# Kernel tuning notes

Hardware: AMD Instinct MI355X
Metric: run time of the kernel (lower is better)

Reference implementation:

```python
import jax, jax.numpy as jnp
import numpy as np

B, DIN, H, NACT = 8192, 1025, 1024, 1026
NHEAD = 513  # npatches + STOP
K = 32       # kR = kS


def _make_seq(key, batch, n, k):
    k_idx, k_len = jax.random.split(key)
    # distinct indices per row: top-k of a random permutation
    perm = jnp.argsort(jax.random.uniform(k_idx, (batch, n)), axis=1)[:, :k]
    seq_len = jax.random.randint(k_len, (batch,), 1, k + 1).astype(jnp.int32)
    mask = jnp.arange(k)[None, :] < seq_len[:, None]
    seq_idx = jnp.where(mask, perm, -1).astype(jnp.int32)
    return seq_idx, seq_len


def setup_inputs() -> dict:
    key = jax.random.key(0)
    ks = jax.random.split(key, 8)
    state = jax.random.normal(ks[0], (B, DIN), dtype=jnp.float32)
    W0 = jax.random.normal(ks[1], (DIN, H), dtype=jnp.float32) * (2.0 / DIN) ** 0.5
    b0 = jnp.zeros((H,), jnp.float32)
    W1 = jax.random.normal(ks[2], (H, H), dtype=jnp.float32) * (2.0 / H) ** 0.5
    b1 = jnp.zeros((H,), jnp.float32)
    W2 = jax.random.normal(ks[3], (H, NACT), dtype=jnp.float32) * 0.01
    b2 = jnp.zeros((NACT,), jnp.float32)
    seq_idx_R, seq_len_R = _make_seq(ks[4], B, NHEAD, K)
    seq_idx_S, seq_len_S = _make_seq(ks[5], B, NHEAD, K)
    return {"state": state, "W0": W0, "b0": b0, "W1": W1, "b1": b1,
            "W2": W2, "b2": b2,
            "seq_idx_R": seq_idx_R, "seq_len_R": seq_len_R,
            "seq_idx_S": seq_idx_S, "seq_len_S": seq_len_S}


def _mlp(state, W0, b0, W1, b1, W2, b2):
    h = jax.nn.relu(state @ W0 + b0)
    h = jax.nn.relu(h @ W1 + b1)
    return h @ W2 + b2  # (B, NACT) logits


def _logprob_entropy_wo_replacement(logits, seq_idx, seq_len):
    # Faithful vectorized version of logprob_entropy_wo_replacement_batched.
    bsz, n = logits.shape
    col = jnp.arange(n)[None, :]
    neg_inf = jnp.float32(-jnp.inf)

    def step(carry, xs):
        remaining, logp, ent = carry          # (B,N) bool, (B,), (B,)
        t, idx_t = xs                          # scalar, (B,)
        active = t < seq_len                   # (B,)
        masked_logits = jnp.where(remaining, logits, neg_inf)
        lp = jax.nn.log_softmax(masked_logits, axis=-1)
        p = jnp.exp(lp)
        mp = jnp.where(remaining, p, 0.0)
        mlp_ = jnp.where(remaining, lp, 0.0)
        ent_step = -jnp.sum(mp * mlp_, axis=-1)
        ent = ent + jnp.where(active, ent_step, 0.0)
        valid = active & (idx_t >= 0)
        idx_safe = jnp.where(valid, idx_t, 0)
        g = jnp.take_along_axis(lp, idx_safe[:, None], axis=1)[:, 0]
        logp = logp + jnp.where(valid, g, 0.0)
        hit = (col == idx_safe[:, None]) & valid[:, None]
        remaining = remaining & ~hit
        return (remaining, logp, ent), None

    init = (jnp.ones((bsz, n), bool), jnp.zeros((bsz,), jnp.float32),
            jnp.zeros((bsz,), jnp.float32))
    ts = jnp.arange(seq_idx.shape[1], dtype=jnp.int32)
    (_, logp, ent), _ = jax.lax.scan(step, init, (ts, seq_idx.T))
    return logp, ent


def reference(state, W0, b0, W1, b1, W2, b2,
              seq_idx_R, seq_len_R, seq_idx_S, seq_len_S):
    x = _mlp(state, W0, b0, W1, b1, W2, b2)
    logpR, entR = _logprob_entropy_wo_replacement(x[:, :NHEAD], seq_idx_R, seq_len_R)
    logpS, entS = _logprob_entropy_wo_replacement(x[:, NHEAD:NHEAD + NHEAD], seq_idx_S, seq_len_S)
    # rows: [total logprob, total entropy] as in get_log_prob's (logpR+logpS, entR+entS)
    return jnp.stack([logpR + logpS, entR + entS], axis=0)  # (2, B)
```

## Files before the change

kernel.cpp:

```cpp
#include <hip/hip_runtime.h>
#include <cstdint>
#include <cstddef>

#define BATCH 8192
#define DIN   1025
#define HID   1024
#define NACT  1026
#define NHEAD 513
#define KSEL  32
#define KP0   1088
#define LGN   1024

typedef unsigned short u16;
typedef short bf16x8 __attribute__((ext_vector_type(8)));
typedef float f32x4 __attribute__((ext_vector_type(4)));

__device__ __forceinline__ u16 f2bf(float f) {
  unsigned u = __float_as_uint(f);
  u += 0x7fff + ((u >> 16) & 1);
  return (u16)(u >> 16);
}
__device__ __forceinline__ float bf2f(u16 h) {
  return __uint_as_float((unsigned)h << 16);
}

__device__ __forceinline__ void async_cp16(const u16* g, u16* l) {
  __builtin_amdgcn_global_load_lds((const __attribute__((address_space(1))) void*)g,
                                   (__attribute__((address_space(3))) void*)l,
                                   16, 0, 0);
}

__global__ __launch_bounds__(512) void k_cvt(const float* __restrict__ state,
    const float* __restrict__ W0, const float* __restrict__ W1,
    const float* __restrict__ W2,
    u16* __restrict__ As, u16* __restrict__ W0t, u16* __restrict__ W1t,
    u16* __restrict__ W2t, u16* __restrict__ W2c) {
  const int tid = threadIdx.x;
  const int b = blockIdx.x;
  {
    int i = b * 512 + tid;
    const int QPR = KP0 / 4;
    int r = i / QPR, c4 = (i - r * QPR) * 4;
    const float* src = state + (size_t)r * DIN + c4;
    ushort4 o;
    if (c4 + 3 < DIN) {
      o.x = f2bf(src[0]); o.y = f2bf(src[1]); o.z = f2bf(src[2]); o.w = f2bf(src[3]);
    } else {
      o.x = (c4 + 0 < DIN) ? f2bf(src[0]) : 0;
      o.y = (c4 + 1 < DIN) ? f2bf(src[1]) : 0;
      o.z = (c4 + 2 < DIN) ? f2bf(src[2]) : 0;
      o.w = (c4 + 3 < DIN) ? f2bf(src[3]) : 0;
    }
    *(ushort4*)(As + (size_t)r * KP0 + c4) = o;
  }
  if (b >= 3137) return;
  if (b == 3136) {
    for (int e = tid; e < 2048; e += 512) {
      int j = e >> 10, k = e & 1023;
      W2c[e] = f2bf(W2[(size_t)k * NACT + 1024 + j]);
    }
    return;
  }
  const float* W; u16* Wt; int K, ldW, Kp, tt = b;
  if (tt < 1088)      { W = W0; Wt = W0t; K = DIN; ldW = HID;  Kp = KP0; }
  else if (tt < 2112) { tt -= 1088; W = W1; Wt = W1t; K = HID; ldW = HID;  Kp = HID; }
  else                { tt -= 2112; W = W2; Wt = W2t; K = HID; ldW = NACT; Kp = HID; }
  int n0 = (tt & 31) * 32, k0 = (tt >> 5) * 32;
  __shared__ float tile[32][33];
  const int tx = tid & 31, ty = tid >> 5;
#pragma unroll
  for (int i = 0; i < 32; i += 16) {
    int k = k0 + ty + i;
    tile[ty + i][tx] = (k < K) ? W[(size_t)k * ldW + n0 + tx] : 0.f;
  }
  __syncthreads();
#pragma unroll
  for (int i = 0; i < 32; i += 16)
    Wt[(size_t)(n0 + ty + i) * Kp + k0 + tx] = f2bf(tile[tx][ty + i]);
}

template<bool RELU, int K>
__global__ __launch_bounds__(512, 1)
void gemm_bt(const u16* __restrict__ A, const u16* __restrict__ Bt,
             const float* __restrict__ bias, u16* __restrict__ Cout, int ldc)
{
  __shared__ __align__(16) u16 lds[73728];

  const int d = blockIdx.x;
  const int wg    = (d & 7) * 32 + (d >> 3);
  const int mtile = wg >> 3;
  const int ntile = wg & 7;
  const size_t bm = (size_t)mtile * 256;
  const size_t bn = (size_t)ntile * 128;

  const int tid  = threadIdx.x;
  const int wave = tid >> 6;
  const int lane = tid & 63;
  const int waveM = wave >> 1, waveN = wave & 1;
  const int lr = lane & 15, lq = lane >> 4;
  const int xr = lr & 7;

  const int row0 = tid >> 3;
  const int g_   = (tid & 7) ^ ((tid >> 3) & 7);
  const u16* gA0 = A  + (bm + row0)       * (size_t)K + g_ * 8;
  const u16* gA1 = A  + (bm + row0 + 64)  * (size_t)K + g_ * 8;
  const u16* gA2 = A  + (bm + row0 + 128) * (size_t)K + g_ * 8;
  const u16* gA3 = A  + (bm + row0 + 192) * (size_t)K + g_ * 8;
  const u16* gB0 = Bt + (bn + row0)       * (size_t)K + g_ * 8;
  const u16* gB1 = Bt + (bn + row0 + 64)  * (size_t)K + g_ * 8;

  auto stage = [&](int k0, int wb) {
    u16* a = lds + wb * 24576 + wave * 512;
    u16* b = a + 16384;
    async_cp16(gA0 + k0, a);
    async_cp16(gA1 + k0, a + 4096);
    async_cp16(gA2 + k0, a + 8192);
    async_cp16(gA3 + k0, a + 12288);
    async_cp16(gB0 + k0, b);
    async_cp16(gB1 + k0, b + 4096);
  };

  const int offA = (waveM * 64 + lr) * 64;
  const int offB = 16384 + (waveN * 64 + lr) * 64;
  const int s0 = ( lq      ^ xr) * 8;
  const int s1 = ((4 | lq) ^ xr) * 8;

  f32x4 acc[4][4] = {};
  bf16x8 af[4], bfr[4];

  const int NIT = K / 64;
  stage(0, 0);
  stage(64, 1);
  asm volatile("s_waitcnt vmcnt(6)" ::: "memory");
  __builtin_amdgcn_s_barrier();

  int rb = 0;
  for (int t = 0; t < NIT; ++t) {
    const int ro = rb * 24576;
    const bool pf = (t + 2 < NIT);

#pragma unroll
    for (int nf = 0; nf < 4; ++nf) bfr[nf] = *(const bf16x8*)(lds + ro + offB + nf * 1024 + s0);
#pragma unroll
    for (int mf = 0; mf < 4; ++mf) af[mf]  = *(const bf16x8*)(lds + ro + offA + mf * 1024 + s0);
    if (pf) {
      int wb = rb - 1; if (wb < 0) wb = 2;
      stage((t + 2) * 64, wb);
    }
    __builtin_amdgcn_s_barrier();
    asm volatile("s_waitcnt lgkmcnt(0)" ::: "memory");
    __builtin_amdgcn_sched_barrier(0);
    __builtin_amdgcn_s_setprio(1);
#pragma unroll
    for (int mf = 0; mf < 4; ++mf)
#pragma unroll
      for (int nf = 0; nf < 4; ++nf)
        acc[mf][nf] = __builtin_amdgcn_mfma_f32_16x16x32_bf16(af[mf], bfr[nf], acc[mf][nf], 0, 0, 0);
    __builtin_amdgcn_s_setprio(0);
    __builtin_amdgcn_s_barrier();

#pragma unroll
    for (int nf = 0; nf < 4; ++nf) bfr[nf] = *(const bf16x8*)(lds + ro + offB + nf * 1024 + s1);
#pragma unroll
    for (int mf = 0; mf < 4; ++mf) af[mf]  = *(const bf16x8*)(lds + ro + offA + mf * 1024 + s1);
    __builtin_amdgcn_s_barrier();
    asm volatile("s_waitcnt lgkmcnt(0)" ::: "memory");
    __builtin_amdgcn_sched_barrier(0);
    __builtin_amdgcn_s_setprio(1);
#pragma unroll
    for (int mf = 0; mf < 4; ++mf)
#pragma unroll
      for (int nf = 0; nf < 4; ++nf)
        acc[mf][nf] = __builtin_amdgcn_mfma_f32_16x16x32_bf16(af[mf], bfr[nf], acc[mf][nf], 0, 0, 0);
    __builtin_amdgcn_s_setprio(0);
    if (pf)               asm volatile("s_waitcnt vmcnt(6)" ::: "memory");
    else if (t + 1 < NIT) asm volatile("s_waitcnt vmcnt(0)" ::: "memory");
    __builtin_amdgcn_s_barrier();

    rb = (rb == 2) ? 0 : rb + 1;
  }

#pragma unroll
  for (int mf = 0; mf < 4; ++mf) {
    size_t rw = bm + waveM * 64 + mf * 16 + lq * 4;
#pragma unroll
    for (int nf = 0; nf < 4; ++nf) {
      int col = (int)bn + waveN * 64 + nf * 16 + lr;
      float bv = bias[col];
#pragma unroll
      for (int r = 0; r < 4; ++r) {
        float v = acc[mf][nf][r] + bv;
        if (RELU) v = fmaxf(v, 0.f);
        Cout[(rw + r) * (size_t)ldc + col] = f2bf(v);
      }
    }
  }
}

__global__ __launch_bounds__(512) void k_sample(const u16* __restrict__ lgts,
    const u16* __restrict__ h2, const u16* __restrict__ W2c,
    const float* __restrict__ b2,
    const int* __restrict__ idxR, const int* __restrict__ lenR,
    const int* __restrict__ idxS, const int* __restrict__ lenS,
    float* __restrict__ out) {
  __shared__ float shf[16];
  const int tid = threadIdx.x;
  const int w = tid >> 6, lane = tid & 63;
  const int grp = w & 1, pair = w >> 1;
  const int row = blockIdx.x * 4 + pair;
  const u16* base = lgts + (size_t)row * LGN + (grp ? NHEAD : 0);
  const int* sidx = (grp ? idxS : idxR) + (size_t)row * KSEL;
  const int slen  = (grp ? lenS : lenR)[row];

  float x1024 = 0.f, x1025 = 0.f;
  if (grp) {
    const bf16x8* hp  = (const bf16x8*)(h2 + (size_t)row * HID + lane * 16);
    const bf16x8* w0p = (const bf16x8*)(W2c + lane * 16);
    const bf16x8* w1p = (const bf16x8*)(W2c + 1024 + lane * 16);
    bf16x8 hv0 = hp[0],  hv1 = hp[1];
    bf16x8 a0  = w0p[0], a1  = w0p[1];
    bf16x8 c0  = w1p[0], c1  = w1p[1];
    float d0 = 0.f, d1 = 0.f;
#pragma unroll
    for (int j = 0; j < 8; ++j) {
      float h0 = bf2f((u16)hv0[j]);
      float h1 = bf2f((u16)hv1[j]);
      d0 += h0 * bf2f((u16)a0[j]) + h1 * bf2f((u16)a1[j]);
      d1 += h0 * bf2f((u16)c0[j]) + h1 * bf2f((u16)c1[j]);
    }
#pragma unroll
    for (int dd = 32; dd; dd >>= 1) { d0 += __shfl_xor(d0, dd, 64); d1 += __shfl_xor(d1, dd, 64); }
    x1024 = d0 + b2[1024];
    x1025 = d1 + b2[1025];
  }

  const u16* chunk = lgts + (size_t)row * LGN + (grp ? 512 : 0) + lane * 8;
  bf16x8 raw = *(const bf16x8*)chunk;
  float v[8];
#pragma unroll
  for (int j = 0; j < 8; ++j) v[j] = bf2f((u16)raw[j]);
  if (grp && lane == 0) v[0] = -3.4e38f;

  float xa = -3.4e38f; int has_xa = 0;
  if (!grp && lane == 0)  { xa = bf2f(base[512]); has_xa = 1; }
  if (grp  && lane == 63) { xa = x1024;           has_xa = 1; }
  if (grp  && lane == 0)  { xa = x1025;           has_xa = 1; }

  float m = -3.4e38f;
#pragma unroll
  for (int j = 0; j < 8; ++j) m = fmaxf(m, v[j]);
  if (has_xa) m = fmaxf(m, xa);
#pragma unroll
  for (int dd = 32; dd; dd >>= 1) m = fmaxf(m, __shfl_xor(m, dd, 64));

  float S = 0.f, T = 0.f;
#pragma unroll
  for (int j = 0; j < 8; ++j) {
    float e = __expf(v[j] - m);
    S += e; T += e * v[j];
  }
  if (has_xa) { float e = __expf(xa - m); S += e; T += e * xa; }
#pragma unroll
  for (int dd = 32; dd; dd >>= 1) { S += __shfl_xor(S, dd, 64); T += __shfl_xor(T, dd, 64); }

  float e = 0.f, ex = 0.f, xt = 0.f;
  int active = (lane < KSEL) && (lane < slen);
  int valid = 0;
  if (active) {
    int id = sidx[lane];
    if (id >= 0) {
      valid = 1;
      if (grp && id >= 511) xt = (id == 511) ? x1024 : x1025;
      else                  xt = bf2f(base[id]);
      e  = __expf(xt - m);
      ex = e * xt;
    }
  }
  float pe = e, pex = ex;
#pragma unroll
  for (int dd = 1; dd < 32; dd <<= 1) {
    float qa = __shfl_up(pe, dd, 64);
    float qb = __shfl_up(pex, dd, 64);
    if (lane >= dd) { pe += qa; pex += qb; }
  }
  float lp = 0.f, en = 0.f;
  if (active) {
    float St = S - (pe - e);
    float Tt = T - (pex - ex);
    float logZ = m + __logf(St);
    en = logZ - Tt / St;
    if (valid) lp = xt - logZ;
  }
#pragma unroll
  for (int dd = 32; dd; dd >>= 1) { lp += __shfl_xor(lp, dd, 64); en += __shfl_xor(en, dd, 64); }

  if (lane == 0) { shf[w * 2] = lp; shf[w * 2 + 1] = en; }
  __syncthreads();
  if (lane == 0 && grp == 0) {
    out[row]         = shf[pair * 4] + shf[pair * 4 + 2];
    out[BATCH + row] = shf[pair * 4 + 1] + shf[pair * 4 + 3];
  }
}

extern "C" void kernel_launch(void* const* d_in, const int* in_sizes, int n_in,
                              void* d_out, int out_size, void* d_ws, size_t ws_size,
                              hipStream_t stream) {
  (void)in_sizes; (void)n_in; (void)out_size; (void)ws_size;
  const float* state = (const float*)d_in[0];
  const float* W0 = (const float*)d_in[1];
  const float* b0 = (const float*)d_in[2];
  const float* W1 = (const float*)d_in[3];
  const float* b1 = (const float*)d_in[4];
  const float* W2 = (const float*)d_in[5];
  const float* b2 = (const float*)d_in[6];
  const int* idxR = (const int*)d_in[7];
  const int* lenR = (const int*)d_in[8];
  const int* idxS = (const int*)d_in[9];
  const int* lenS = (const int*)d_in[10];
  float* out = (float*)d_out;

  char* ws = (char*)d_ws;
  size_t off = 0;
  auto alloc = [&](size_t bytes) -> char* {
    char* p = ws + off;
    off = (off + bytes + 255) & ~(size_t)255;
    return p;
  };
  u16* As   = (u16*)alloc((size_t)BATCH * KP0 * 2);
  u16* W0t  = (u16*)alloc((size_t)HID * KP0 * 2);
  u16* W1t  = (u16*)alloc((size_t)HID * HID * 2);
  u16* W2t  = (u16*)alloc((size_t)HID * LGN * 2);
  u16* W2c  = (u16*)alloc((size_t)2 * 1024 * 2);
  u16* h1   = (u16*)alloc((size_t)BATCH * HID * 2);
  u16* h2   = (u16*)alloc((size_t)BATCH * HID * 2);
  u16* lgts = (u16*)alloc((size_t)BATCH * LGN * 2);

  k_cvt<<<4352, 512, 0, stream>>>(state, W0, W1, W2, As, W0t, W1t, W2t, W2c);

  gemm_bt<true,  KP0><<<256, 512, 0, stream>>>(As, W0t, b0, h1,   HID);
  gemm_bt<true,  HID><<<256, 512, 0, stream>>>(h1, W1t, b1, h2,   HID);
  gemm_bt<false, HID><<<256, 512, 0, stream>>>(h2, W2t, b2, lgts, LGN);

  k_sample<<<2048, 512, 0, stream>>>(lgts, h2, W2c, b2, idxR, lenR, idxS, lenS, out);
}
```

Before: 185.0 us.

## Enlarge GEMM tiles to 256x256 with a four-stage k32 async pipeline

```diff
diff --git a/kernel.cpp b/kernel.cpp
--- a/kernel.cpp
+++ b/kernel.cpp
@@ -84,69 +84,63 @@
 void gemm_bt(const u16* __restrict__ A, const u16* __restrict__ Bt,
              const float* __restrict__ bias, u16* __restrict__ Cout, int ldc)
 {
-  __shared__ __align__(16) u16 lds[73728];
+  __shared__ __align__(16) u16 lds[65536];
 
   const int d = blockIdx.x;
-  const int wg    = (d & 7) * 32 + (d >> 3);
-  const int mtile = wg >> 3;
-  const int ntile = wg & 7;
+  const int wg    = (d & 7) * 16 + (d >> 3);
+  const int mtile = wg >> 2;
+  const int ntile = wg & 3;
   const size_t bm = (size_t)mtile * 256;
-  const size_t bn = (size_t)ntile * 128;
+  const size_t bn = (size_t)ntile * 256;
 
   const int tid  = threadIdx.x;
   const int wave = tid >> 6;
   const int lane = tid & 63;
-  const int waveM = wave >> 1, waveN = wave & 1;
+  const int waveM = wave >> 2, waveN = wave & 3;
   const int lr = lane & 15, lq = lane >> 4;
-  const int xr = lr & 7;
-
-  const int row0 = tid >> 3;
-  const int g_   = (tid & 7) ^ ((tid >> 3) & 7);
+
+  const int row0 = tid >> 2;
+  const int g_   = (tid & 3) ^ ((tid >> 2) & 3) ^ ((tid >> 4) & 3);
   const u16* gA0 = A  + (bm + row0)       * (size_t)K + g_ * 8;
-  const u16* gA1 = A  + (bm + row0 + 64)  * (size_t)K + g_ * 8;
-  const u16* gA2 = A  + (bm + row0 + 128) * (size_t)K + g_ * 8;
-  const u16* gA3 = A  + (bm + row0 + 192) * (size_t)K + g_ * 8;
+  const u16* gA1 = A  + (bm + row0 + 128) * (size_t)K + g_ * 8;
   const u16* gB0 = Bt + (bn + row0)       * (size_t)K + g_ * 8;
-  const u16* gB1 = Bt + (bn + row0 + 64)  * (size_t)K + g_ * 8;
-
-  auto stage = [&](int k0, int wb) {
-    u16* a = lds + wb * 24576 + wave * 512;
-    u16* b = a + 16384;
+  const u16* gB1 = Bt + (bn + row0 + 128) * (size_t)K + g_ * 8;
+
+  auto stageA = [&](int k0, int wo) {
+    u16* a = lds + wo + wave * 512;
     async_cp16(gA0 + k0, a);
     async_cp16(gA1 + k0, a + 4096);
-    async_cp16(gA2 + k0, a + 8192);
-    async_cp16(gA3 + k0, a + 12288);
+  };
+  auto stageB = [&](int k0, int wo) {
+    u16* b = lds + wo + 8192 + wave * 512;
     async_cp16(gB0 + k0, b);
     async_cp16(gB1 + k0, b + 4096);
   };
 
-  const int offA = (waveM * 64 + lr) * 64;
-  const int offB = 16384 + (waveN * 64 + lr) * 64;
-  const int s0 = ( lq      ^ xr) * 8;
-  const int s1 = ((4 | lq) ^ xr) * 8;
-
-  f32x4 acc[4][4] = {};
+  const int offA = (waveM * 128 + lr) * 32;
+  const int offB = 8192 + (waveN * 64 + lr) * 32;
+  const int s_   = ((lq ^ (lr & 3) ^ ((lr >> 2) & 3))) * 8;
+
+  f32x4 acc[8][4] = {};
   bf16x8 af[4], bfr[4];
 
-  const int NIT = K / 64;
-  stage(0, 0);
-  stage(64, 1);
-  asm volatile("s_waitcnt vmcnt(6)" ::: "memory");
+  const int NIT = K / 32;
+  stageA(0, 0);          stageB(0, 0);
+  stageA(32, 16384);     stageB(32, 16384);
+  stageA(64, 32768);     stageB(64, 32768);
+  asm volatile("s_waitcnt vmcnt(8)" ::: "memory");
   __builtin_amdgcn_s_barrier();
 
-  int rb = 0;
+  int ro = 0;
   for (int t = 0; t < NIT; ++t) {
-    const int ro = rb * 24576;
-    const bool pf = (t + 2 < NIT);
-
-#pragma unroll
-    for (int nf = 0; nf < 4; ++nf) bfr[nf] = *(const bf16x8*)(lds + ro + offB + nf * 1024 + s0);
-#pragma unroll
-    for (int mf = 0; mf < 4; ++mf) af[mf]  = *(const bf16x8*)(lds + ro + offA + mf * 1024 + s0);
-    if (pf) {
-      int wb = rb - 1; if (wb < 0) wb = 2;
-      stage((t + 2) * 64, wb);
-    }
+    const int wo = (ro + 3 * 16384) & 65535;
+    const bool pf = (t + 3 < NIT);
+
+#pragma unroll
+    for (int nf = 0; nf < 4; ++nf) bfr[nf] = *(const bf16x8*)(lds + ro + offB + nf * 512 + s_);
+#pragma unroll
+    for (int mf = 0; mf < 4; ++mf) af[mf]  = *(const bf16x8*)(lds + ro + offA + mf * 512 + s_);
+    if (pf) stageA((t + 3) * 32, wo);
     __builtin_amdgcn_s_barrier();
     asm volatile("s_waitcnt lgkmcnt(0)" ::: "memory");
     __builtin_amdgcn_sched_barrier(0);
@@ -160,9 +154,8 @@
     __builtin_amdgcn_s_barrier();
 
 #pragma unroll
-    for (int nf = 0; nf < 4; ++nf) bfr[nf] = *(const bf16x8*)(lds + ro + offB + nf * 1024 + s1);
-#pragma unroll
-    for (int mf = 0; mf < 4; ++mf) af[mf]  = *(const bf16x8*)(lds + ro + offA + mf * 1024 + s1);
+    for (int mf = 0; mf < 4; ++mf) af[mf] = *(const bf16x8*)(lds + ro + offA + (mf + 4) * 512 + s_);
+    if (pf) stageB((t + 3) * 32, wo);
     __builtin_amdgcn_s_barrier();
     asm volatile("s_waitcnt lgkmcnt(0)" ::: "memory");
     __builtin_amdgcn_sched_barrier(0);
@@ -171,18 +164,19 @@
     for (int mf = 0; mf < 4; ++mf)
 #pragma unroll
       for (int nf = 0; nf < 4; ++nf)
-        acc[mf][nf] = __builtin_amdgcn_mfma_f32_16x16x32_bf16(af[mf], bfr[nf], acc[mf][nf], 0, 0, 0);
+        acc[mf + 4][nf] = __builtin_amdgcn_mfma_f32_16x16x32_bf16(af[mf], bfr[nf], acc[mf + 4][nf], 0, 0, 0);
     __builtin_amdgcn_s_setprio(0);
-    if (pf)               asm volatile("s_waitcnt vmcnt(6)" ::: "memory");
-    else if (t + 1 < NIT) asm volatile("s_waitcnt vmcnt(0)" ::: "memory");
+    if (pf)                asm volatile("s_waitcnt vmcnt(8)" ::: "memory");
+    else if (t + 3 == NIT) asm volatile("s_waitcnt vmcnt(4)" ::: "memory");
+    else if (t + 2 == NIT) asm volatile("s_waitcnt vmcnt(0)" ::: "memory");
     __builtin_amdgcn_s_barrier();
 
-    rb = (rb == 2) ? 0 : rb + 1;
-  }
-
-#pragma unroll
-  for (int mf = 0; mf < 4; ++mf) {
-    size_t rw = bm + waveM * 64 + mf * 16 + lq * 4;
+    ro = (ro + 16384) & 65535;
+  }
+
+#pragma unroll
+  for (int mf = 0; mf < 8; ++mf) {
+    size_t rw = bm + waveM * 128 + mf * 16 + lq * 4;
 #pragma unroll
     for (int nf = 0; nf < 4; ++nf) {
       int col = (int)bn + waveN * 64 + nf * 16 + lr;
@@ -337,9 +331,9 @@
 
   k_cvt<<<4352, 512, 0, stream>>>(state, W0, W1, W2, As, W0t, W1t, W2t, W2c);
 
-  gemm_bt<true,  KP0><<<256, 512, 0, stream>>>(As, W0t, b0, h1,   HID);
-  gemm_bt<true,  HID><<<256, 512, 0, stream>>>(h1, W1t, b1, h2,   HID);
-  gemm_bt<false, HID><<<256, 512, 0, stream>>>(h2, W2t, b2, lgts, LGN);
+  gemm_bt<true,  KP0><<<128, 512, 0, stream>>>(As, W0t, b0, h1,   HID);
+  gemm_bt<true,  HID><<<128, 512, 0, stream>>>(h1, W1t, b1, h2,   HID);
+  gemm_bt<false, HID><<<128, 512, 0, stream>>>(h2, W2t, b2, lgts, LGN);
 
   k_sample<<<2048, 512, 0, stream>>>(lgts, h2, W2c, b2, idxR, lenR, idxS, lenS, out);
 }
```

Result: slower. 226.7 us (+22.5%).

## Use 4 waves with 128x64 per-wave tiles in GEMM kernels

Applied to the files above, without the earlier changes.

```diff
diff --git a/kernel.cpp b/kernel.cpp
--- a/kernel.cpp
+++ b/kernel.cpp
@@ -80,7 +80,7 @@
 }
 
 template<bool RELU, int K>
-__global__ __launch_bounds__(512, 1)
+__global__ __launch_bounds__(256, 1)
 void gemm_bt(const u16* __restrict__ A, const u16* __restrict__ Bt,
              const float* __restrict__ bias, u16* __restrict__ Cout, int ldc)
 {
@@ -98,55 +98,57 @@
   const int lane = tid & 63;
   const int waveM = wave >> 1, waveN = wave & 1;
   const int lr = lane & 15, lq = lane >> 4;
-  const int xr = lr & 7;
+  const int xr = lane & 7;
 
   const int row0 = tid >> 3;
   const int g_   = (tid & 7) ^ ((tid >> 3) & 7);
-  const u16* gA0 = A  + (bm + row0)       * (size_t)K + g_ * 8;
-  const u16* gA1 = A  + (bm + row0 + 64)  * (size_t)K + g_ * 8;
-  const u16* gA2 = A  + (bm + row0 + 128) * (size_t)K + g_ * 8;
-  const u16* gA3 = A  + (bm + row0 + 192) * (size_t)K + g_ * 8;
-  const u16* gB0 = Bt + (bn + row0)       * (size_t)K + g_ * 8;
-  const u16* gB1 = Bt + (bn + row0 + 64)  * (size_t)K + g_ * 8;
-
-  auto stage = [&](int k0, int wb) {
-    u16* a = lds + wb * 24576 + wave * 512;
-    u16* b = a + 16384;
-    async_cp16(gA0 + k0, a);
-    async_cp16(gA1 + k0, a + 4096);
-    async_cp16(gA2 + k0, a + 8192);
-    async_cp16(gA3 + k0, a + 12288);
-    async_cp16(gB0 + k0, b);
-    async_cp16(gB1 + k0, b + 4096);
+  const u16* gA = A  + (bm + row0) * (size_t)K + g_ * 8;
+  const u16* gB = Bt + (bn + row0) * (size_t)K + g_ * 8;
+
+  auto stage_part = [&](int k0, int wo, int p) {
+    u16* a = lds + wo + wave * 512;
+    u16* b = lds + wo + 16384 + wave * 512;
+    if (p == 0) {
+#pragma unroll
+      for (int k = 0; k < 3; ++k) async_cp16(gA + (size_t)(k * 32) * K + k0, a + k * 2048);
+    } else if (p == 1) {
+#pragma unroll
+      for (int k = 3; k < 6; ++k) async_cp16(gA + (size_t)(k * 32) * K + k0, a + k * 2048);
+    } else if (p == 2) {
+#pragma unroll
+      for (int k = 6; k < 8; ++k) async_cp16(gA + (size_t)(k * 32) * K + k0, a + k * 2048);
+      async_cp16(gB + k0, b);
+    } else {
+#pragma unroll
+      for (int k = 1; k < 4; ++k) async_cp16(gB + (size_t)(k * 32) * K + k0, b + k * 2048);
+    }
   };
 
-  const int offA = (waveM * 64 + lr) * 64;
+  const int offA = (waveM * 128 + lr) * 64;
   const int offB = 16384 + (waveN * 64 + lr) * 64;
   const int s0 = ( lq      ^ xr) * 8;
   const int s1 = ((4 | lq) ^ xr) * 8;
 
-  f32x4 acc[4][4] = {};
+  f32x4 acc[8][4] = {};
   bf16x8 af[4], bfr[4];
 
   const int NIT = K / 64;
-  stage(0, 0);
-  stage(64, 1);
-  asm volatile("s_waitcnt vmcnt(6)" ::: "memory");
+  stage_part(0, 0, 0);  stage_part(0, 0, 1);  stage_part(0, 0, 2);  stage_part(0, 0, 3);
+  stage_part(64, 24576, 0); stage_part(64, 24576, 1); stage_part(64, 24576, 2); stage_part(64, 24576, 3);
+  asm volatile("s_waitcnt vmcnt(12)" ::: "memory");
   __builtin_amdgcn_s_barrier();
 
-  int rb = 0;
+  int ro = 0;
   for (int t = 0; t < NIT; ++t) {
-    const int ro = rb * 24576;
+    int wo = ro + 49152; if (wo >= 73728) wo -= 73728;
+    const int kn = (t + 2) * 64;
     const bool pf = (t + 2 < NIT);
 
 #pragma unroll
     for (int nf = 0; nf < 4; ++nf) bfr[nf] = *(const bf16x8*)(lds + ro + offB + nf * 1024 + s0);
 #pragma unroll
     for (int mf = 0; mf < 4; ++mf) af[mf]  = *(const bf16x8*)(lds + ro + offA + mf * 1024 + s0);
-    if (pf) {
-      int wb = rb - 1; if (wb < 0) wb = 2;
-      stage((t + 2) * 64, wb);
-    }
+    if (pf) stage_part(kn, wo, 0);
     __builtin_amdgcn_s_barrier();
     asm volatile("s_waitcnt lgkmcnt(0)" ::: "memory");
     __builtin_amdgcn_sched_barrier(0);
@@ -160,9 +162,8 @@
     __builtin_amdgcn_s_barrier();
 
 #pragma unroll
-    for (int nf = 0; nf < 4; ++nf) bfr[nf] = *(const bf16x8*)(lds + ro + offB + nf * 1024 + s1);
-#pragma unroll
-    for (int mf = 0; mf < 4; ++mf) af[mf]  = *(const bf16x8*)(lds + ro + offA + mf * 1024 + s1);
+    for (int mf = 0; mf < 4; ++mf) af[mf] = *(const bf16x8*)(lds + ro + offA + (mf + 4) * 1024 + s0);
+    if (pf) stage_part(kn, wo, 1);
     __builtin_amdgcn_s_barrier();
     asm volatile("s_waitcnt lgkmcnt(0)" ::: "memory");
     __builtin_amdgcn_sched_barrier(0);
@@ -171,18 +172,50 @@
     for (int mf = 0; mf < 4; ++mf)
 #pragma unroll
       for (int nf = 0; nf < 4; ++nf)
+        acc[mf + 4][nf] = __builtin_amdgcn_mfma_f32_16x16x32_bf16(af[mf], bfr[nf], acc[mf + 4][nf], 0, 0, 0);
+    __builtin_amdgcn_s_setprio(0);
+    __builtin_amdgcn_s_barrier();
+
+#pragma unroll
+    for (int nf = 0; nf < 4; ++nf) bfr[nf] = *(const bf16x8*)(lds + ro + offB + nf * 1024 + s1);
+#pragma unroll
+    for (int mf = 0; mf < 4; ++mf) af[mf]  = *(const bf16x8*)(lds + ro + offA + mf * 1024 + s1);
+    if (pf) stage_part(kn, wo, 2);
+    __builtin_amdgcn_s_barrier();
+    asm volatile("s_waitcnt lgkmcnt(0)" ::: "memory");
+    __builtin_amdgcn_sched_barrier(0);
+    __builtin_amdgcn_s_setprio(1);
+#pragma unroll
+    for (int mf = 0; mf < 4; ++mf)
+#pragma unroll
+      for (int nf = 0; nf < 4; ++nf)
         acc[mf][nf] = __builtin_amdgcn_mfma_f32_16x16x32_bf16(af[mf], bfr[nf], acc[mf][nf], 0, 0, 0);
     __builtin_amdgcn_s_setprio(0);
-    if (pf)               asm volatile("s_waitcnt vmcnt(6)" ::: "memory");
-    else if (t + 1 < NIT) asm volatile("s_waitcnt vmcnt(0)" ::: "memory");
-    __builtin_amdgcn_s_barrier();
-
-    rb = (rb == 2) ? 0 : rb + 1;
-  }
-
-#pragma unroll
-  for (int mf = 0; mf < 4; ++mf) {
-    size_t rw = bm + waveM * 64 + mf * 16 + lq * 4;
+    __builtin_amdgcn_s_barrier();
+
+#pragma unroll
+    for (int mf = 0; mf < 4; ++mf) af[mf] = *(const bf16x8*)(lds + ro + offA + (mf + 4) * 1024 + s1);
+    if (pf) stage_part(kn, wo, 3);
+    __builtin_amdgcn_s_barrier();
+    asm volatile("s_waitcnt lgkmcnt(0)" ::: "memory");
+    __builtin_amdgcn_sched_barrier(0);
+    __builtin_amdgcn_s_setprio(1);
+#pragma unroll
+    for (int mf = 0; mf < 4; ++mf)
+#pragma unroll
+      for (int nf = 0; nf < 4; ++nf)
+        acc[mf + 4][nf] = __builtin_amdgcn_mfma_f32_16x16x32_bf16(af[mf], bfr[nf], acc[mf + 4][nf], 0, 0, 0);
+    __builtin_amdgcn_s_setprio(0);
+    if (pf)                asm volatile("s_waitcnt vmcnt(12)" ::: "memory");
+    else if (t + 1 < NIT)  asm volatile("s_waitcnt vmcnt(0)"  ::: "memory");
+    __builtin_amdgcn_s_barrier();
+
+    ro += 24576; if (ro >= 73728) ro = 0;
+  }
+
+#pragma unroll
+  for (int mf = 0; mf < 8; ++mf) {
+    size_t rw = bm + waveM * 128 + mf * 16 + lq * 4;
 #pragma unroll
     for (int nf = 0; nf < 4; ++nf) {
       int col = (int)bn + waveN * 64 + nf * 16 + lr;
@@ -337,9 +370,9 @@
 
   k_cvt<<<4352, 512, 0, stream>>>(state, W0, W1, W2, As, W0t, W1t, W2t, W2c);
 
-  gemm_bt<true,  KP0><<<256, 512, 0, stream>>>(As, W0t, b0, h1,   HID);
-  gemm_bt<true,  HID><<<256, 512, 0, stream>>>(h1, W1t, b1, h2,   HID);
-  gemm_bt<false, HID><<<256, 512, 0, stream>>>(h2, W2t, b2, lgts, LGN);
+  gemm_bt<true,  KP0><<<256, 256, 0, stream>>>(As, W0t, b0, h1,   HID);
+  gemm_bt<true,  HID><<<256, 256, 0, stream>>>(h1, W1t, b1, h2,   HID);
+  gemm_bt<false, HID><<<256, 256, 0, stream>>>(h2, W2t, b2, lgts, LGN);
 
   k_sample<<<2048, 512, 0, stream>>>(lgts, h2, W2c, b2, idxR, lenR, idxS, lenS, out);
 }
```

Result: slower. 202.7 us (+9.5%).
